# Performance work log

Hardware: AMD Instinct MI355X
Metric: run time of the kernel (lower is better)

## Reference

```python
import jax, jax.numpy as jnp
import numpy as np

GRID = 32          # grid_size -> N = 1024 patches
NPT = 1            # num_prefix_tokens
SCALE = 8.0        # sqrt(dim_head=64)
EPS = 1e-5         # nn.LayerNorm default eps


def _ln(x, g, b):
    m = jnp.mean(x, axis=-1, keepdims=True)
    v = jnp.var(x, axis=-1, keepdims=True)
    return (x - m) / jnp.sqrt(v + EPS) * g + b


def setup_inputs() -> dict:
    key = jax.random.key(0)
    ks = jax.random.split(key, 12)
    B, T, D, Dh = 32, GRID * GRID + NPT, 768, 64
    s = 0.02
    return {
        "x": jax.random.normal(ks[0], (B, T, D), jnp.float32),
        "Wq": jax.random.normal(ks[1], (D, Dh), jnp.float32) * s,
        "Wk": jax.random.normal(ks[2], (D, Dh), jnp.float32) * s,
        "Wv": jax.random.normal(ks[3], (D, Dh), jnp.float32) * s,
        "gq": jnp.ones((Dh,), jnp.float32),
        "bq": jnp.zeros((Dh,), jnp.float32),
        "gk": jnp.ones((Dh,), jnp.float32),
        "bk": jnp.zeros((Dh,), jnp.float32),
        "Wsig": jax.random.normal(ks[4], (Dh, 2), jnp.float32) * s,
        "bsig": jnp.zeros((2,), jnp.float32),
        "Wa": jax.random.normal(ks[5], (Dh, 1), jnp.float32) * s,
        "ba": jnp.zeros((1,), jnp.float32),
    }


def reference(x, Wq, Wk, Wv, gq, bq, gk, bk, Wsig, bsig, Wa, ba):
    # x: [B, T, D] with T = GRID^2 + NPT
    q = _ln(x @ Wq, gq, bq)            # [B, T, Dh]
    k = _ln(x @ Wk, gk, bk)            # [B, T, Dh]
    v = x @ Wv                          # [B, T, Dh]

    q_patch = q[:, NPT:, :]             # [B, N, Dh]
    alpha = jax.nn.softplus(q_patch @ Wa + ba)[..., 0]   # [B, N]
    sig = jax.nn.sigmoid(q_patch @ Wsig + bsig)          # [B, N, 2]
    sx, sy = sig[..., 0], sig[..., 1]                     # [B, N] each

    # patch-grid relative displacements (vectorized replacement of the
    # O(N^2) python double loop)
    ii, jj = jnp.meshgrid(jnp.arange(GRID), jnp.arange(GRID), indexing="ij")
    coords = jnp.stack([ii.ravel(), jj.ravel()], axis=-1).astype(jnp.float32)  # [N,2]=(y,x)
    dy = coords[:, None, 0] - coords[None, :, 0]          # [N, N]
    dx = coords[:, None, 1] - coords[None, :, 1]          # [N, N]

    # Gaussian bias: G[b,p,q] = exp(-dx^2/(2 sx[b,p]^2) - dy^2/(2 sy[b,p]^2))
    G = jnp.exp(-(dx * dx) / (2.0 * sx[:, :, None] ** 2)
                - (dy * dy) / (2.0 * sy[:, :, None] ** 2))  # [B, N, N]
    S = alpha[:, :, None] * G                               # [B, N, N]

    sim = jnp.einsum("bqd,bkd->bqk", q, k)                  # [B, T, T]
    sim = sim.at[:, NPT:, NPT:].add(S)

    probs = jax.nn.softmax(sim / SCALE, axis=-1)
    return probs @ v                                         # [B, T, Dh]
```

## Files before the change

### kernel.cpp

```cpp
#include <hip/hip_runtime.h>
#include <hip/hip_bf16.h>
#include <math.h>

#define BDIM 32
#define TDIM 1025
#define DDIM 768
#define GRIDW 32
#define TPATCH 1024
#define SCALE 8.0f
#define EPSLN 1e-5f
#define NROW (BDIM * TDIM)
#define VTLD 1088
#define LDP  72
#define NTILES 17

typedef __attribute__((ext_vector_type(8))) short short8v;
typedef __attribute__((ext_vector_type(4))) float f32x4;

__device__ __forceinline__ unsigned short f2bf(float f) {
    unsigned int u = __float_as_uint(f);
    u += 0x7FFFu + ((u >> 16) & 1u);
    return (unsigned short)(u >> 16);
}

__device__ __forceinline__ short8v pack8(float4 a, float4 b) {
    union { short8v v; unsigned short s[8]; } u;
    u.s[0] = f2bf(a.x); u.s[1] = f2bf(a.y); u.s[2] = f2bf(a.z); u.s[3] = f2bf(a.w);
    u.s[4] = f2bf(b.x); u.s[5] = f2bf(b.y); u.s[6] = f2bf(b.z); u.s[7] = f2bf(b.w);
    return u.v;
}

template<int CTRL>
__device__ __forceinline__ float dpp_f(float x) {
    return __int_as_float(__builtin_amdgcn_update_dpp(
        __float_as_int(x), __float_as_int(x), CTRL, 0xF, 0xF, true));
}
__device__ __forceinline__ float red16_max(float x) {
    x = fmaxf(x, dpp_f<0xB1>(x));
    x = fmaxf(x, dpp_f<0x4E>(x));
    x = fmaxf(x, dpp_f<0x124>(x));
    x = fmaxf(x, dpp_f<0x128>(x));
    return x;
}
__device__ __forceinline__ float red16_sum(float x) {
    x += dpp_f<0xB1>(x);
    x += dpp_f<0x4E>(x);
    x += dpp_f<0x124>(x);
    x += dpp_f<0x128>(x);
    return x;
}

__global__ __launch_bounds__(256) void prep_w_kernel(
    const float* __restrict__ Wq, const float* __restrict__ Wk,
    const float* __restrict__ Wv, unsigned short* __restrict__ wT)
{
    const int c = blockIdx.x;
    const float* W = (c < 64) ? Wq : (c < 128) ? Wk : Wv;
    const int cc = c & 63;
    for (int k = threadIdx.x; k < DDIM; k += 256)
        wT[(size_t)c * DDIM + k] = f2bf(W[(size_t)k * 64 + cc]);
}

__global__ __launch_bounds__(256) void qkv_tile_kernel(
    const float* __restrict__ x, const unsigned short* __restrict__ wT,
    const float* __restrict__ gq, const float* __restrict__ bq,
    const float* __restrict__ gk, const float* __restrict__ bk,
    const float* __restrict__ Wsig, const float* __restrict__ bsig,
    const float* __restrict__ Wa, const float* __restrict__ ba,
    unsigned short* __restrict__ qb, unsigned short* __restrict__ kb,
    unsigned short* __restrict__ vb,
    float* __restrict__ a8, float* __restrict__ isx, float* __restrict__ isy)
{
    __shared__ unsigned short As[2][64][LDP];
    __shared__ unsigned short Bs[2][192][LDP];

    const int t  = threadIdx.x;
    const int wv = t >> 6;
    const int ln = t & 63;
    const int lq = ln >> 4;
    const int lr = ln & 15;
    const int tok0 = blockIdx.x * 64;

    const float* la_ptr[2];
    const unsigned short* lb_ptr[6];
#pragma unroll
    for (int j = 0; j < 2; ++j) {
        int lin = t + 256 * j;
        la_ptr[j] = x + (size_t)min(tok0 + (lin >> 3), NROW - 1) * DDIM + (lin & 7) * 8;
    }
#pragma unroll
    for (int j = 0; j < 6; ++j) {
        int lin = t + 256 * j;
        lb_ptr[j] = wT + (size_t)(lin >> 3) * DDIM + (lin & 7) * 8;
    }

    float4  raf[2][2];
    short8v rbv[6];

#define QLOAD(K0)                                                              \
    do {                                                                       \
        _Pragma("unroll") for (int j = 0; j < 2; ++j) {                        \
            raf[j][0] = *(const float4*)(la_ptr[j] + (K0));                    \
            raf[j][1] = *(const float4*)(la_ptr[j] + (K0) + 4);                \
        }                                                                      \
        _Pragma("unroll") for (int j = 0; j < 6; ++j)                          \
            rbv[j] = *(const short8v*)(lb_ptr[j] + (K0));                      \
    } while (0)

#define QSTORE(BUF)                                                            \
    do {                                                                       \
        _Pragma("unroll") for (int j = 0; j < 2; ++j) {                        \
            int lin = t + 256 * j;                                             \
            *(short8v*)&As[BUF][lin >> 3][(lin & 7) * 8] =                     \
                pack8(raf[j][0], raf[j][1]);                                   \
        }                                                                      \
        _Pragma("unroll") for (int j = 0; j < 6; ++j) {                        \
            int lin = t + 256 * j;                                             \
            *(short8v*)&Bs[BUF][lin >> 3][(lin & 7) * 8] = rbv[j];             \
        }                                                                      \
    } while (0)

    f32x4 acc[12];
#pragma unroll
    for (int ni = 0; ni < 12; ++ni) acc[ni] = (f32x4){0.f, 0.f, 0.f, 0.f};

    QLOAD(0);
    QSTORE(0);
    __syncthreads();

#pragma unroll
    for (int ks = 0; ks < 12; ++ks) {
        const int buf = ks & 1;
        if (ks + 1 < 12) QLOAD((ks + 1) * 64);
        short8v af0 = *(const short8v*)&As[buf][wv * 16 + lr][lq * 8];
        short8v af1 = *(const short8v*)&As[buf][wv * 16 + lr][32 + lq * 8];
#pragma unroll
        for (int ni = 0; ni < 12; ++ni) {
            short8v bf0 = *(const short8v*)&Bs[buf][16 * ni + lr][lq * 8];
            acc[ni] = __builtin_amdgcn_mfma_f32_16x16x32_bf16(af0, bf0, acc[ni], 0, 0, 0);
            short8v bf1 = *(const short8v*)&Bs[buf][16 * ni + lr][32 + lq * 8];
            acc[ni] = __builtin_amdgcn_mfma_f32_16x16x32_bf16(af1, bf1, acc[ni], 0, 0, 0);
        }
        if (ks + 1 < 12) QSTORE(buf ^ 1);
        __syncthreads();
    }
#undef QLOAD
#undef QSTORE

    float gqv[4], bqv[4], gkv[4], bkv[4], wav[4], ws0[4], ws1[4];
#pragma unroll
    for (int ni = 0; ni < 4; ++ni) {
        int c = lr + 16 * ni;
        gqv[ni] = gq[c]; bqv[ni] = bq[c];
        gkv[ni] = gk[c]; bkv[ni] = bk[c];
        wav[ni] = Wa[c];
        ws0[ni] = Wsig[2 * c];
        ws1[ni] = Wsig[2 * c + 1];
    }
    const float ba0 = ba[0], bs0 = bsig[0], bs1 = bsig[1];

#pragma unroll
    for (int reg = 0; reg < 4; ++reg) {
        const int tokr = tok0 + wv * 16 + lq * 4 + reg;

        float s1 = 0.f, s2 = 0.f;
#pragma unroll
        for (int ni = 0; ni < 4; ++ni) {
            float v = acc[ni][reg];
            s1 += v; s2 += v * v;
        }
        s1 = red16_sum(s1);
        s2 = red16_sum(s2);
        float mean = s1 * (1.f / 64.f);
        float var  = s2 * (1.f / 64.f) - mean * mean;
        float rstd = rsqrtf(var + EPSLN);
        float qn[4];
#pragma unroll
        for (int ni = 0; ni < 4; ++ni)
            qn[ni] = (acc[ni][reg] - mean) * rstd * gqv[ni] + bqv[ni];

        s1 = 0.f; s2 = 0.f;
#pragma unroll
        for (int ni = 0; ni < 4; ++ni) {
            float v = acc[4 + ni][reg];
            s1 += v; s2 += v * v;
        }
        s1 = red16_sum(s1);
        s2 = red16_sum(s2);
        mean = s1 * (1.f / 64.f);
        var  = s2 * (1.f / 64.f) - mean * mean;
        rstd = rsqrtf(var + EPSLN);
        float kn[4];
#pragma unroll
        for (int ni = 0; ni < 4; ++ni)
            kn[ni] = (acc[4 + ni][reg] - mean) * rstd * gkv[ni] + bkv[ni];

        float da = 0.f, d0 = 0.f, d1 = 0.f;
#pragma unroll
        for (int ni = 0; ni < 4; ++ni) {
            da += qn[ni] * wav[ni];
            d0 += qn[ni] * ws0[ni];
            d1 += qn[ni] * ws1[ni];
        }
        da = red16_sum(da);
        d0 = red16_sum(d0);
        d1 = red16_sum(d1);

        if (tokr < NROW) {
            size_t base = (size_t)tokr * 64;
            int bidx = tokr / TDIM;
            int ti   = tokr - bidx * TDIM;
#pragma unroll
            for (int ni = 0; ni < 4; ++ni) {
                int c = lr + 16 * ni;
                qb[base + c] = f2bf(qn[ni]);
                kb[base + c] = f2bf(kn[ni]);
                vb[base + c] = f2bf(acc[8 + ni][reg]);
            }
            if (lr == 0 && ti >= 1) {
                int p = bidx * TPATCH + ti - 1;
                float av = da + ba0;
                float sp = (av > 20.f) ? av : log1pf(__expf(av));
                a8[p] = sp * (1.f / SCALE);
                float sx = 1.f / (1.f + __expf(-(d0 + bs0)));
                float sy = 1.f / (1.f + __expf(-(d1 + bs1)));
                isx[p] = 0.5f / (sx * sx);
                isy[p] = 0.5f / (sy * sy);
            }
        }
    }
}

__global__ __launch_bounds__(256) void vtrans_kernel(
    const unsigned short* __restrict__ vb, unsigned short* __restrict__ vT)
{
    __shared__ unsigned short tile[64][LDP];
    const int t  = threadIdx.x;
    const int bb = blockIdx.y;
    const int t0 = blockIdx.x * 64;

#pragma unroll
    for (int it = 0; it < 2; ++it) {
        int lin = t + it * 256;
        int tok = lin >> 3;
        int d0  = (lin & 7) * 8;
        short8v v8 = {0, 0, 0, 0, 0, 0, 0, 0};
        if (t0 + tok < TDIM)
            v8 = *(const short8v*)&vb[((size_t)bb * TDIM + t0 + tok) * 64 + d0];
        union { short8v v; unsigned short s[8]; } u; u.v = v8;
#pragma unroll
        for (int j = 0; j < 8; ++j) tile[d0 + j][tok] = u.s[j];
    }
    __syncthreads();

    const int dh = t >> 2;
    const int ch = t & 3;
    short8v o0 = *(const short8v*)&tile[dh][ch * 16];
    short8v o1 = *(const short8v*)&tile[dh][ch * 16 + 8];
    size_t dst = ((size_t)bb * 64 + dh) * VTLD + t0 + ch * 16;
    *(short8v*)&vT[dst]     = o0;
    *(short8v*)&vT[dst + 8] = o1;
}

__global__ __launch_bounds__(256) void attn_mfma_kernel(
    const unsigned short* __restrict__ qb, const unsigned short* __restrict__ kb,
    const unsigned short* __restrict__ vT,
    const float* __restrict__ a8, const float* __restrict__ isx,
    const float* __restrict__ isy, float* __restrict__ out)
{
    __shared__ unsigned short Ks[2][64][LDP];
    __shared__ unsigned short Vt[2][64][LDP];
    __shared__ unsigned short Pt[4][16][LDP];

    const int t  = threadIdx.x;
    const int wv = t >> 6;
    const int ln = t & 63;
    const int lq = ln >> 4;
    const int lr = ln & 15;
    const int bb = blockIdx.y;
    const int q0 = blockIdx.x * 64;

    const int qrow = min(q0 + wv * 16 + lr, TDIM - 1);
    const size_t qbase = ((size_t)bb * TDIM + qrow) * 64;
    const short8v aq0 = *(const short8v*)&qb[qbase + lq * 8];
    const short8v aq1 = *(const short8v*)&qb[qbase + 32 + lq * 8];

    float a8q[4], sxq[4], syq[4], qpy[4], qpx[4];
    bool  hasS[4];
#pragma unroll
    for (int reg = 0; reg < 4; ++reg) {
        int qg = q0 + wv * 16 + lq * 4 + reg;
        hasS[reg] = false;
        a8q[reg] = 0.f; sxq[reg] = 0.f; syq[reg] = 0.f; qpy[reg] = 0.f; qpx[reg] = 0.f;
        if (qg >= 1 && qg < TDIM) {
            int qp = qg - 1;
            hasS[reg] = true;
            a8q[reg] = a8 [bb * TPATCH + qp];
            sxq[reg] = isx[bb * TPATCH + qp];
            syq[reg] = isy[bb * TPATCH + qp];
            qpy[reg] = (float)(qp >> 5);
            qpx[reg] = (float)(qp & 31);
        }
    }

    float m[4]  = {-1e30f, -1e30f, -1e30f, -1e30f};
    float l[4]  = {0.f, 0.f, 0.f, 0.f};
    f32x4 oacc[4];
#pragma unroll
    for (int ni = 0; ni < 4; ++ni) oacc[ni] = (f32x4){0.f, 0.f, 0.f, 0.f};

    const int sk_row = t >> 3;
    const int sk_d0  = (t & 7) * 8;
    short8v rk[2], rv[2];

#define ALOAD(KT0)                                                             \
    do {                                                                       \
        _Pragma("unroll") for (int it = 0; it < 2; ++it) {                     \
            int key = sk_row + 32 * it;                                        \
            int kg  = (KT0) + key;                                             \
            rk[it] = (kg < TDIM)                                               \
                ? *(const short8v*)&kb[((size_t)bb * TDIM + kg) * 64 + sk_d0]  \
                : (short8v){0, 0, 0, 0, 0, 0, 0, 0};                           \
            rv[it] = *(const short8v*)&vT[((size_t)bb * 64 + key) * VTLD +     \
                                          (KT0) + sk_d0];                      \
        }                                                                      \
    } while (0)

#define ASTORE(BUF)                                                            \
    do {                                                                       \
        _Pragma("unroll") for (int it = 0; it < 2; ++it) {                     \
            *(short8v*)&Ks[BUF][sk_row + 32 * it][sk_d0] = rk[it];             \
            *(short8v*)&Vt[BUF][sk_row + 32 * it][sk_d0] = rv[it];             \
        }                                                                      \
    } while (0)

    ALOAD(0);
    ASTORE(0);
    __syncthreads();

    for (int tile = 0; tile < NTILES; ++tile) {
        const int kt0 = tile * 64;
        const int buf = tile & 1;
        if (tile + 1 < NTILES) ALOAD(kt0 + 64);

        f32x4 sac[4];
#pragma unroll
        for (int ni = 0; ni < 4; ++ni) sac[ni] = (f32x4){0.f, 0.f, 0.f, 0.f};
#pragma unroll
        for (int ni = 0; ni < 4; ++ni) {
            short8v b0 = *(const short8v*)&Ks[buf][16 * ni + lr][lq * 8];
            short8v b1 = *(const short8v*)&Ks[buf][16 * ni + lr][32 + lq * 8];
            sac[ni] = __builtin_amdgcn_mfma_f32_16x16x32_bf16(aq0, b0, sac[ni], 0, 0, 0);
            sac[ni] = __builtin_amdgcn_mfma_f32_16x16x32_bf16(aq1, b1, sac[ni], 0, 0, 0);
        }

#pragma unroll
        for (int ni = 0; ni < 4; ++ni) {
            int key = kt0 + 16 * ni + lr;
            int kp  = key - 1;
            float ky = (float)(kp >> 5);
            float kx = (float)(kp & 31);
            bool kvalid = (key >= 1) && (key < TDIM);
#pragma unroll
            for (int reg = 0; reg < 4; ++reg) {
                float z = sac[ni][reg] * (1.f / SCALE);
                if (kvalid && hasS[reg]) {
                    float dy = qpy[reg] - ky;
                    float dx = qpx[reg] - kx;
                    z += a8q[reg] * __expf(-(dx * dx * sxq[reg] + dy * dy * syq[reg]));
                }
                if (key >= TDIM) z = -1e30f;
                sac[ni][reg] = z;
            }
        }

        float scf[4];
#pragma unroll
        for (int reg = 0; reg < 4; ++reg) {
            float mx = fmaxf(fmaxf(sac[0][reg], sac[1][reg]),
                             fmaxf(sac[2][reg], sac[3][reg]));
            mx = red16_max(mx);
            float mn = fmaxf(m[reg], mx);
            scf[reg] = __expf(m[reg] - mn);
            m[reg] = mn;
            float ts = 0.f;
#pragma unroll
            for (int ni = 0; ni < 4; ++ni) {
                float pp = __expf(sac[ni][reg] - mn);
                sac[ni][reg] = pp;
                ts += pp;
            }
            ts = red16_sum(ts);
            l[reg] = l[reg] * scf[reg] + ts;
        }
#pragma unroll
        for (int ni = 0; ni < 4; ++ni)
#pragma unroll
            for (int reg = 0; reg < 4; ++reg)
                oacc[ni][reg] *= scf[reg];

#pragma unroll
        for (int ni = 0; ni < 4; ++ni)
#pragma unroll
            for (int reg = 0; reg < 4; ++reg)
                Pt[wv][lq * 4 + reg][16 * ni + lr] = f2bf(sac[ni][reg]);

#pragma unroll
        for (int ks = 0; ks < 2; ++ks) {
            short8v pa = *(const short8v*)&Pt[wv][lr][ks * 32 + lq * 8];
#pragma unroll
            for (int ni = 0; ni < 4; ++ni) {
                short8v bv = *(const short8v*)&Vt[buf][16 * ni + lr][ks * 32 + lq * 8];
                oacc[ni] = __builtin_amdgcn_mfma_f32_16x16x32_bf16(pa, bv, oacc[ni], 0, 0, 0);
            }
        }

        if (tile + 1 < NTILES) ASTORE(buf ^ 1);
        __syncthreads();
    }
#undef ALOAD
#undef ASTORE

#pragma unroll
    for (int reg = 0; reg < 4; ++reg) {
        int qg = q0 + wv * 16 + lq * 4 + reg;
        if (qg < TDIM) {
            float rl = 1.f / l[reg];
#pragma unroll
            for (int ni = 0; ni < 4; ++ni)
                out[((size_t)bb * TDIM + qg) * 64 + 16 * ni + lr] = oacc[ni][reg] * rl;
        }
    }
}

extern "C" void kernel_launch(void* const* d_in, const int* in_sizes, int n_in,
                              void* d_out, int out_size, void* d_ws, size_t ws_size,
                              hipStream_t stream)
{
    const float* x    = (const float*)d_in[0];
    const float* Wq   = (const float*)d_in[1];
    const float* Wk   = (const float*)d_in[2];
    const float* Wv   = (const float*)d_in[3];
    const float* gq   = (const float*)d_in[4];
    const float* bq   = (const float*)d_in[5];
    const float* gk   = (const float*)d_in[6];
    const float* bk   = (const float*)d_in[7];
    const float* Wsig = (const float*)d_in[8];
    const float* bsig = (const float*)d_in[9];
    const float* Wa   = (const float*)d_in[10];
    const float* ba   = (const float*)d_in[11];
    float* out = (float*)d_out;

    char* w = (char*)d_ws;
    const size_t NQ = (size_t)NROW * 64;
    unsigned short* qb = (unsigned short*)w;   w += NQ * 2;
    unsigned short* kb = (unsigned short*)w;   w += NQ * 2;
    unsigned short* vb = (unsigned short*)w;   w += NQ * 2;
    unsigned short* vT = (unsigned short*)w;   w += (size_t)BDIM * 64 * VTLD * 2;
    float* a8  = (float*)w;                    w += (size_t)BDIM * TPATCH * 4;
    float* isx = (float*)w;                    w += (size_t)BDIM * TPATCH * 4;
    float* isy = (float*)w;                    w += (size_t)BDIM * TPATCH * 4;
    unsigned short* wT = (unsigned short*)w;   w += (size_t)192 * DDIM * 2;

    hipLaunchKernelGGL(prep_w_kernel, dim3(192), dim3(256), 0, stream,
                       Wq, Wk, Wv, wT);

    const int nblk1 = (NROW + 63) / 64;
    hipLaunchKernelGGL(qkv_tile_kernel, dim3(nblk1), dim3(256), 0, stream,
                       x, wT, gq, bq, gk, bk, Wsig, bsig, Wa, ba,
                       qb, kb, vb, a8, isx, isy);

    hipLaunchKernelGGL(vtrans_kernel, dim3(17, BDIM), dim3(256), 0, stream,
                       vb, vT);

    hipLaunchKernelGGL(attn_mfma_kernel, dim3(17, BDIM), dim3(256), 0, stream,
                       qb, kb, vT, a8, isx, isy, out);
}
```

Measured before the change: 108.5 us.

## Halve QKV GEMM K-tile and double-buffer register prefetch with lighter barriers

The QKV projection GEMM now steps through K in 32-wide slices instead of 64, using narrower shared tiles. Two alternating register prefetch sets keep a global load two slices ahead of the MFMA compute. Both the QKV and attention kernels replace __syncthreads with a barrier that waits only on LDS counters and adds a scheduling fence, so outstanding global loads can stay in flight across it. The aim is better overlap of global memory traffic with MFMA work, at the cost of twice as many barriers in the GEMM and more live registers.

```diff
diff --git a/kernel.cpp b/kernel.cpp
--- a/kernel.cpp
+++ b/kernel.cpp
@@ -12,6 +12,7 @@
 #define NROW (BDIM * TDIM)
 #define VTLD 1088
 #define LDP  72
+#define LDQ  40
 #define NTILES 17
 
 typedef __attribute__((ext_vector_type(8))) short short8v;
@@ -23,11 +24,16 @@
     return (unsigned short)(u >> 16);
 }
 
-__device__ __forceinline__ short8v pack8(float4 a, float4 b) {
-    union { short8v v; unsigned short s[8]; } u;
-    u.s[0] = f2bf(a.x); u.s[1] = f2bf(a.y); u.s[2] = f2bf(a.z); u.s[3] = f2bf(a.w);
-    u.s[4] = f2bf(b.x); u.s[5] = f2bf(b.y); u.s[6] = f2bf(b.z); u.s[7] = f2bf(b.w);
-    return u.v;
+__device__ __forceinline__ ushort4 pack4(float4 a) {
+    ushort4 r;
+    r.x = f2bf(a.x); r.y = f2bf(a.y); r.z = f2bf(a.z); r.w = f2bf(a.w);
+    return r;
+}
+
+__device__ __forceinline__ void wg_barrier() {
+    asm volatile("s_waitcnt lgkmcnt(0)" ::: "memory");
+    __builtin_amdgcn_s_barrier();
+    __builtin_amdgcn_sched_barrier(0);
 }
 
 template<int CTRL>
@@ -71,8 +77,8 @@
     unsigned short* __restrict__ vb,
     float* __restrict__ a8, float* __restrict__ isx, float* __restrict__ isy)
 {
-    __shared__ unsigned short As[2][64][LDP];
-    __shared__ unsigned short Bs[2][192][LDP];
+    __shared__ unsigned short As[2][64][LDQ];
+    __shared__ unsigned short Bs[2][192][LDQ];
 
     const int t  = threadIdx.x;
     const int wv = t >> 6;
@@ -81,71 +87,87 @@
     const int lr = ln & 15;
     const int tok0 = blockIdx.x * 64;
 
-    const float* la_ptr[2];
-    const unsigned short* lb_ptr[6];
-#pragma unroll
-    for (int j = 0; j < 2; ++j) {
-        int lin = t + 256 * j;
-        la_ptr[j] = x + (size_t)min(tok0 + (lin >> 3), NROW - 1) * DDIM + (lin & 7) * 8;
-    }
-#pragma unroll
-    for (int j = 0; j < 6; ++j) {
-        int lin = t + 256 * j;
-        lb_ptr[j] = wT + (size_t)(lin >> 3) * DDIM + (lin & 7) * 8;
-    }
-
-    float4  raf[2][2];
-    short8v rbv[6];
-
-#define QLOAD(K0)                                                              \
-    do {                                                                       \
-        _Pragma("unroll") for (int j = 0; j < 2; ++j) {                        \
-            raf[j][0] = *(const float4*)(la_ptr[j] + (K0));                    \
-            raf[j][1] = *(const float4*)(la_ptr[j] + (K0) + 4);                \
+    const int ar0 = t >> 3,          as0 = (t & 7) * 4;
+    const int ar1 = (t + 256) >> 3,  as1 = ((t + 256) & 7) * 4;
+    const float* la0 = x + (size_t)min(tok0 + ar0, NROW - 1) * DDIM + as0;
+    const float* la1 = x + (size_t)min(tok0 + ar1, NROW - 1) * DDIM + as1;
+    const int br0 = t >> 2,          bs0 = (t & 3) * 8;
+    const int br1 = (t + 256) >> 2,  bs1 = ((t + 256) & 3) * 8;
+    const int br2 = (t + 512) >> 2,  bs2 = ((t + 512) & 3) * 8;
+    const unsigned short* lb0 = wT + (size_t)br0 * DDIM + bs0;
+    const unsigned short* lb1 = wT + (size_t)br1 * DDIM + bs1;
+    const unsigned short* lb2 = wT + (size_t)br2 * DDIM + bs2;
+
+    float4  raA0, raA1, raB0, raB1;
+    short8v rbA0, rbA1, rbA2, rbB0, rbB1, rbB2;
+
+#define LOAD_SET_A(K0)                                                         \
+    do {                                                                       \
+        raA0 = *(const float4*)(la0 + (K0));                                   \
+        raA1 = *(const float4*)(la1 + (K0));                                   \
+        rbA0 = *(const short8v*)(lb0 + (K0));                                  \
+        rbA1 = *(const short8v*)(lb1 + (K0));                                  \
+        rbA2 = *(const short8v*)(lb2 + (K0));                                  \
+    } while (0)
+#define LOAD_SET_B(K0)                                                         \
+    do {                                                                       \
+        raB0 = *(const float4*)(la0 + (K0));                                   \
+        raB1 = *(const float4*)(la1 + (K0));                                   \
+        rbB0 = *(const short8v*)(lb0 + (K0));                                  \
+        rbB1 = *(const short8v*)(lb1 + (K0));                                  \
+        rbB2 = *(const short8v*)(lb2 + (K0));                                  \
+    } while (0)
+#define STORE_SET_A()                                                          \
+    do {                                                                       \
+        *(ushort4*)&As[0][ar0][as0] = pack4(raA0);                             \
+        *(ushort4*)&As[0][ar1][as1] = pack4(raA1);                             \
+        *(short8v*)&Bs[0][br0][bs0] = rbA0;                                    \
+        *(short8v*)&Bs[0][br1][bs1] = rbA1;                                    \
+        *(short8v*)&Bs[0][br2][bs2] = rbA2;                                    \
+    } while (0)
+#define STORE_SET_B()                                                          \
+    do {                                                                       \
+        *(ushort4*)&As[1][ar0][as0] = pack4(raB0);                             \
+        *(ushort4*)&As[1][ar1][as1] = pack4(raB1);                             \
+        *(short8v*)&Bs[1][br0][bs0] = rbB0;                                    \
+        *(short8v*)&Bs[1][br1][bs1] = rbB1;                                    \
+        *(short8v*)&Bs[1][br2][bs2] = rbB2;                                    \
+    } while (0)
+#define COMPUTE(BUF)                                                           \
+    do {                                                                       \
+        short8v af = *(const short8v*)&As[BUF][wv * 16 + lr][lq * 8];          \
+        _Pragma("unroll") for (int ni = 0; ni < 12; ++ni) {                    \
+            short8v bf = *(const short8v*)&Bs[BUF][16 * ni + lr][lq * 8];      \
+            acc[ni] = __builtin_amdgcn_mfma_f32_16x16x32_bf16(af, bf,          \
+                                                              acc[ni], 0, 0, 0); \
         }                                                                      \
-        _Pragma("unroll") for (int j = 0; j < 6; ++j)                          \
-            rbv[j] = *(const short8v*)(lb_ptr[j] + (K0));                      \
-    } while (0)
-
-#define QSTORE(BUF)                                                            \
-    do {                                                                       \
-        _Pragma("unroll") for (int j = 0; j < 2; ++j) {                        \
-            int lin = t + 256 * j;                                             \
-            *(short8v*)&As[BUF][lin >> 3][(lin & 7) * 8] =                     \
-                pack8(raf[j][0], raf[j][1]);                                   \
-        }                                                                      \
-        _Pragma("unroll") for (int j = 0; j < 6; ++j) {                        \
-            int lin = t + 256 * j;                                             \
-            *(short8v*)&Bs[BUF][lin >> 3][(lin & 7) * 8] = rbv[j];             \
-        }                                                                      \
     } while (0)
 
     f32x4 acc[12];
 #pragma unroll
     for (int ni = 0; ni < 12; ++ni) acc[ni] = (f32x4){0.f, 0.f, 0.f, 0.f};
 
-    QLOAD(0);
-    QSTORE(0);
-    __syncthreads();
-
-#pragma unroll
-    for (int ks = 0; ks < 12; ++ks) {
-        const int buf = ks & 1;
-        if (ks + 1 < 12) QLOAD((ks + 1) * 64);
-        short8v af0 = *(const short8v*)&As[buf][wv * 16 + lr][lq * 8];
-        short8v af1 = *(const short8v*)&As[buf][wv * 16 + lr][32 + lq * 8];
-#pragma unroll
-        for (int ni = 0; ni < 12; ++ni) {
-            short8v bf0 = *(const short8v*)&Bs[buf][16 * ni + lr][lq * 8];
-            acc[ni] = __builtin_amdgcn_mfma_f32_16x16x32_bf16(af0, bf0, acc[ni], 0, 0, 0);
-            short8v bf1 = *(const short8v*)&Bs[buf][16 * ni + lr][32 + lq * 8];
-            acc[ni] = __builtin_amdgcn_mfma_f32_16x16x32_bf16(af1, bf1, acc[ni], 0, 0, 0);
-        }
-        if (ks + 1 < 12) QSTORE(buf ^ 1);
-        __syncthreads();
-    }
-#undef QLOAD
-#undef QSTORE
+    LOAD_SET_A(0);
+    LOAD_SET_B(32);
+    STORE_SET_A();
+    wg_barrier();
+
+#pragma unroll
+    for (int ks = 0; ks < 24; ks += 2) {
+        if (ks + 2 < 24) LOAD_SET_A((ks + 2) * 32);
+        COMPUTE(0);
+        STORE_SET_B();
+        wg_barrier();
+        if (ks + 3 < 24) LOAD_SET_B((ks + 3) * 32);
+        COMPUTE(1);
+        if (ks + 2 < 24) STORE_SET_A();
+        wg_barrier();
+    }
+#undef LOAD_SET_A
+#undef LOAD_SET_B
+#undef STORE_SET_A
+#undef STORE_SET_B
+#undef COMPUTE
 
     float gqv[4], bqv[4], gkv[4], bkv[4], wav[4], ws0[4], ws1[4];
 #pragma unroll
@@ -157,7 +179,7 @@
         ws0[ni] = Wsig[2 * c];
         ws1[ni] = Wsig[2 * c + 1];
     }
-    const float ba0 = ba[0], bs0 = bsig[0], bs1 = bsig[1];
+    const float ba0 = ba[0], bs0c = bsig[0], bs1c = bsig[1];
 
 #pragma unroll
     for (int reg = 0; reg < 4; ++reg) {
@@ -222,8 +244,8 @@
                 float av = da + ba0;
                 float sp = (av > 20.f) ? av : log1pf(__expf(av));
                 a8[p] = sp * (1.f / SCALE);
-                float sx = 1.f / (1.f + __expf(-(d0 + bs0)));
-                float sy = 1.f / (1.f + __expf(-(d1 + bs1)));
+                float sx = 1.f / (1.f + __expf(-(d0 + bs0c)));
+                float sy = 1.f / (1.f + __expf(-(d1 + bs1c)));
                 isx[p] = 0.5f / (sx * sx);
                 isy[p] = 0.5f / (sy * sy);
             }
@@ -336,7 +358,7 @@
 
     ALOAD(0);
     ASTORE(0);
-    __syncthreads();
+    wg_barrier();
 
     for (int tile = 0; tile < NTILES; ++tile) {
         const int kt0 = tile * 64;
@@ -416,7 +438,7 @@
         }
 
         if (tile + 1 < NTILES) ASTORE(buf ^ 1);
-        __syncthreads();
+        wg_barrier();
     }
 #undef ALOAD
 #undef ASTORE
```

After: 95.55 us. 12.0% less time.

## Restructure QKV projection into single-wave 32-token blocks without barriers

Applied to the files above, without the earlier changes.

The QKV projection kernel moves from 256-thread blocks over 64 tokens with double-buffered LDS to 64-thread single-wave blocks over 32 tokens. Each wave computes two 16-row M tiles against all 192 output columns with a K step of 32. Because only one wave shares the LDS tiles, the per-step workgroup barriers are removed and a single buffer is enough. This doubles the number of blocks and the re-reads of the weight tile, and relies on each wave covering enough latency on its own. The attention kernel's __syncthreads is also replaced by an explicit lgkmcnt wait, s_barrier and scheduling barrier.

```diff
diff --git a/kernel.cpp b/kernel.cpp
--- a/kernel.cpp
+++ b/kernel.cpp
@@ -12,6 +12,7 @@
 #define NROW (BDIM * TDIM)
 #define VTLD 1088
 #define LDP  72
+#define LDQ  40
 #define NTILES 17
 
 typedef __attribute__((ext_vector_type(8))) short short8v;
@@ -23,11 +24,16 @@
     return (unsigned short)(u >> 16);
 }
 
-__device__ __forceinline__ short8v pack8(float4 a, float4 b) {
-    union { short8v v; unsigned short s[8]; } u;
-    u.s[0] = f2bf(a.x); u.s[1] = f2bf(a.y); u.s[2] = f2bf(a.z); u.s[3] = f2bf(a.w);
-    u.s[4] = f2bf(b.x); u.s[5] = f2bf(b.y); u.s[6] = f2bf(b.z); u.s[7] = f2bf(b.w);
-    return u.v;
+__device__ __forceinline__ ushort4 pack4(float4 a) {
+    ushort4 r;
+    r.x = f2bf(a.x); r.y = f2bf(a.y); r.z = f2bf(a.z); r.w = f2bf(a.w);
+    return r;
+}
+
+__device__ __forceinline__ void wg_barrier() {
+    asm volatile("s_waitcnt lgkmcnt(0)" ::: "memory");
+    __builtin_amdgcn_s_barrier();
+    __builtin_amdgcn_sched_barrier(0);
 }
 
 template<int CTRL>
@@ -61,7 +67,7 @@
         wT[(size_t)c * DDIM + k] = f2bf(W[(size_t)k * 64 + cc]);
 }
 
-__global__ __launch_bounds__(256) void qkv_tile_kernel(
+__global__ __launch_bounds__(64) void qkv_tile_kernel(
     const float* __restrict__ x, const unsigned short* __restrict__ wT,
     const float* __restrict__ gq, const float* __restrict__ bq,
     const float* __restrict__ gk, const float* __restrict__ bk,
@@ -71,78 +77,72 @@
     unsigned short* __restrict__ vb,
     float* __restrict__ a8, float* __restrict__ isx, float* __restrict__ isy)
 {
-    __shared__ unsigned short As[2][64][LDP];
-    __shared__ unsigned short Bs[2][192][LDP];
-
-    const int t  = threadIdx.x;
-    const int wv = t >> 6;
-    const int ln = t & 63;
-    const int lq = ln >> 4;
-    const int lr = ln & 15;
-    const int tok0 = blockIdx.x * 64;
-
-    const float* la_ptr[2];
-    const unsigned short* lb_ptr[6];
-#pragma unroll
-    for (int j = 0; j < 2; ++j) {
-        int lin = t + 256 * j;
-        la_ptr[j] = x + (size_t)min(tok0 + (lin >> 3), NROW - 1) * DDIM + (lin & 7) * 8;
-    }
-#pragma unroll
-    for (int j = 0; j < 6; ++j) {
-        int lin = t + 256 * j;
-        lb_ptr[j] = wT + (size_t)(lin >> 3) * DDIM + (lin & 7) * 8;
-    }
-
-    float4  raf[2][2];
-    short8v rbv[6];
+    __shared__ unsigned short As[32][LDQ];
+    __shared__ unsigned short Bs[192][LDQ];
+
+    const int l  = threadIdx.x;
+    const int lq = l >> 4;
+    const int lr = l & 15;
+    const int tok0 = blockIdx.x * 32;
+
+    const float* aptr[4];
+    int arow[4], aseg[4];
+#pragma unroll
+    for (int j = 0; j < 4; ++j) {
+        int c = l + 64 * j;
+        arow[j] = c >> 3;
+        aseg[j] = (c & 7) * 4;
+        aptr[j] = x + (size_t)(tok0 + arow[j]) * DDIM + aseg[j];
+    }
+    const unsigned short* bptr[12];
+    int brow[12], bseg[12];
+#pragma unroll
+    for (int j = 0; j < 12; ++j) {
+        int c = l + 64 * j;
+        brow[j] = c >> 2;
+        bseg[j] = (c & 3) * 8;
+        bptr[j] = wT + (size_t)brow[j] * DDIM + bseg[j];
+    }
+
+    float4  ra[4];
+    short8v rb[12];
 
 #define QLOAD(K0)                                                              \
     do {                                                                       \
-        _Pragma("unroll") for (int j = 0; j < 2; ++j) {                        \
-            raf[j][0] = *(const float4*)(la_ptr[j] + (K0));                    \
-            raf[j][1] = *(const float4*)(la_ptr[j] + (K0) + 4);                \
-        }                                                                      \
-        _Pragma("unroll") for (int j = 0; j < 6; ++j)                          \
-            rbv[j] = *(const short8v*)(lb_ptr[j] + (K0));                      \
+        _Pragma("unroll") for (int j = 0; j < 4; ++j)                          \
+            ra[j] = *(const float4*)(aptr[j] + (K0));                          \
+        _Pragma("unroll") for (int j = 0; j < 12; ++j)                         \
+            rb[j] = *(const short8v*)(bptr[j] + (K0));                         \
     } while (0)
-
-#define QSTORE(BUF)                                                            \
+#define QSTORE()                                                               \
     do {                                                                       \
-        _Pragma("unroll") for (int j = 0; j < 2; ++j) {                        \
-            int lin = t + 256 * j;                                             \
-            *(short8v*)&As[BUF][lin >> 3][(lin & 7) * 8] =                     \
-                pack8(raf[j][0], raf[j][1]);                                   \
-        }                                                                      \
-        _Pragma("unroll") for (int j = 0; j < 6; ++j) {                        \
-            int lin = t + 256 * j;                                             \
-            *(short8v*)&Bs[BUF][lin >> 3][(lin & 7) * 8] = rbv[j];             \
-        }                                                                      \
+        _Pragma("unroll") for (int j = 0; j < 4; ++j)                          \
+            *(ushort4*)&As[arow[j]][aseg[j]] = pack4(ra[j]);                   \
+        _Pragma("unroll") for (int j = 0; j < 12; ++j)                         \
+            *(short8v*)&Bs[brow[j]][bseg[j]] = rb[j];                          \
     } while (0)
 
-    f32x4 acc[12];
-#pragma unroll
-    for (int ni = 0; ni < 12; ++ni) acc[ni] = (f32x4){0.f, 0.f, 0.f, 0.f};
+    f32x4 acc[2][12];
+#pragma unroll
+    for (int mi = 0; mi < 2; ++mi)
+#pragma unroll
+        for (int ni = 0; ni < 12; ++ni)
+            acc[mi][ni] = (f32x4){0.f, 0.f, 0.f, 0.f};
 
     QLOAD(0);
-    QSTORE(0);
-    __syncthreads();
-
-#pragma unroll
-    for (int ks = 0; ks < 12; ++ks) {
-        const int buf = ks & 1;
-        if (ks + 1 < 12) QLOAD((ks + 1) * 64);
-        short8v af0 = *(const short8v*)&As[buf][wv * 16 + lr][lq * 8];
-        short8v af1 = *(const short8v*)&As[buf][wv * 16 + lr][32 + lq * 8];
+    QSTORE();
+
+    for (int ks = 0; ks < 24; ++ks) {
+        if (ks + 1 < 24) QLOAD((ks + 1) * 32);
+        short8v af0 = *(const short8v*)&As[ 0 + lr][lq * 8];
+        short8v af1 = *(const short8v*)&As[16 + lr][lq * 8];
 #pragma unroll
         for (int ni = 0; ni < 12; ++ni) {
-            short8v bf0 = *(const short8v*)&Bs[buf][16 * ni + lr][lq * 8];
-            acc[ni] = __builtin_amdgcn_mfma_f32_16x16x32_bf16(af0, bf0, acc[ni], 0, 0, 0);
-            short8v bf1 = *(const short8v*)&Bs[buf][16 * ni + lr][32 + lq * 8];
-            acc[ni] = __builtin_amdgcn_mfma_f32_16x16x32_bf16(af1, bf1, acc[ni], 0, 0, 0);
-        }
-        if (ks + 1 < 12) QSTORE(buf ^ 1);
-        __syncthreads();
+            short8v bf = *(const short8v*)&Bs[16 * ni + lr][lq * 8];
+            acc[0][ni] = __builtin_amdgcn_mfma_f32_16x16x32_bf16(af0, bf, acc[0][ni], 0, 0, 0);
+            acc[1][ni] = __builtin_amdgcn_mfma_f32_16x16x32_bf16(af1, bf, acc[1][ni], 0, 0, 0);
+        }
+        if (ks + 1 < 24) QSTORE();
     }
 #undef QLOAD
 #undef QSTORE
@@ -157,16 +157,18 @@
         ws0[ni] = Wsig[2 * c];
         ws1[ni] = Wsig[2 * c + 1];
     }
-    const float ba0 = ba[0], bs0 = bsig[0], bs1 = bsig[1];
-
+    const float ba0 = ba[0], bs0c = bsig[0], bs1c = bsig[1];
+
+#pragma unroll
+    for (int mi = 0; mi < 2; ++mi) {
 #pragma unroll
     for (int reg = 0; reg < 4; ++reg) {
-        const int tokr = tok0 + wv * 16 + lq * 4 + reg;
+        const int tokr = tok0 + mi * 16 + lq * 4 + reg;
 
         float s1 = 0.f, s2 = 0.f;
 #pragma unroll
         for (int ni = 0; ni < 4; ++ni) {
-            float v = acc[ni][reg];
+            float v = acc[mi][ni][reg];
             s1 += v; s2 += v * v;
         }
         s1 = red16_sum(s1);
@@ -177,12 +179,12 @@
         float qn[4];
 #pragma unroll
         for (int ni = 0; ni < 4; ++ni)
-            qn[ni] = (acc[ni][reg] - mean) * rstd * gqv[ni] + bqv[ni];
+            qn[ni] = (acc[mi][ni][reg] - mean) * rstd * gqv[ni] + bqv[ni];
 
         s1 = 0.f; s2 = 0.f;
 #pragma unroll
         for (int ni = 0; ni < 4; ++ni) {
-            float v = acc[4 + ni][reg];
+            float v = acc[mi][4 + ni][reg];
             s1 += v; s2 += v * v;
         }
         s1 = red16_sum(s1);
@@ -193,7 +195,7 @@
         float kn[4];
 #pragma unroll
         for (int ni = 0; ni < 4; ++ni)
-            kn[ni] = (acc[4 + ni][reg] - mean) * rstd * gkv[ni] + bkv[ni];
+            kn[ni] = (acc[mi][4 + ni][reg] - mean) * rstd * gkv[ni] + bkv[ni];
 
         float da = 0.f, d0 = 0.f, d1 = 0.f;
 #pragma unroll
@@ -206,7 +208,7 @@
         d0 = red16_sum(d0);
         d1 = red16_sum(d1);
 
-        if (tokr < NROW) {
+        {
             size_t base = (size_t)tokr * 64;
             int bidx = tokr / TDIM;
             int ti   = tokr - bidx * TDIM;
@@ -215,19 +217,20 @@
                 int c = lr + 16 * ni;
                 qb[base + c] = f2bf(qn[ni]);
                 kb[base + c] = f2bf(kn[ni]);
-                vb[base + c] = f2bf(acc[8 + ni][reg]);
+                vb[base + c] = f2bf(acc[mi][8 + ni][reg]);
             }
             if (lr == 0 && ti >= 1) {
                 int p = bidx * TPATCH + ti - 1;
                 float av = da + ba0;
                 float sp = (av > 20.f) ? av : log1pf(__expf(av));
                 a8[p] = sp * (1.f / SCALE);
-                float sx = 1.f / (1.f + __expf(-(d0 + bs0)));
-                float sy = 1.f / (1.f + __expf(-(d1 + bs1)));
+                float sx = 1.f / (1.f + __expf(-(d0 + bs0c)));
+                float sy = 1.f / (1.f + __expf(-(d1 + bs1c)));
                 isx[p] = 0.5f / (sx * sx);
                 isy[p] = 0.5f / (sy * sy);
             }
         }
+    }
     }
 }
 
@@ -336,7 +339,7 @@
 
     ALOAD(0);
     ASTORE(0);
-    __syncthreads();
+    wg_barrier();
 
     for (int tile = 0; tile < NTILES; ++tile) {
         const int kt0 = tile * 64;
@@ -416,7 +419,7 @@
         }
 
         if (tile + 1 < NTILES) ASTORE(buf ^ 1);
-        __syncthreads();
+        wg_barrier();
     }
 #undef ALOAD
 #undef ASTORE
@@ -465,8 +468,8 @@
     hipLaunchKernelGGL(prep_w_kernel, dim3(192), dim3(256), 0, stream,
                        Wq, Wk, Wv, wT);
 
-    const int nblk1 = (NROW + 63) / 64;
-    hipLaunchKernelGGL(qkv_tile_kernel, dim3(nblk1), dim3(256), 0, stream,
+    const int nblk1 = NROW / 32;
+    hipLaunchKernelGGL(qkv_tile_kernel, dim3(nblk1), dim3(64), 0, stream,
                        x, wT, gq, bq, gk, bk, Wsig, bsig, Wa, ba,
                        qb, kb, vb, a8, isx, isy);
 
```

Measured after the change: 105.4 us (median of 2 runs). 1.03x faster.

## Load x directly into MFMA fragments and stage weights in large LDS chunks

Applied to the files above, without the earlier changes.

The QKV projection kernel no longer stages x through LDS. Each lane loads its own x row segment straight from global memory into registers, converts it to bf16 for the MFMA operand, and prefetches two steps ahead. The weight matrix is staged in three 256-wide K chunks with a single buffer, which cuts the number of barriers from twelve to six, but loads and compute no longer overlap within a chunk. The attention kernel's __syncthreads calls are replaced by a custom barrier that waits only on lgkmcnt and adds a scheduling barrier. That barrier does not wait on outstanding global loads.

```diff
diff --git a/kernel.cpp b/kernel.cpp
--- a/kernel.cpp
+++ b/kernel.cpp
@@ -12,6 +12,8 @@
 #define NROW (BDIM * TDIM)
 #define VTLD 1088
 #define LDP  72
+#define BKC  256
+#define LDB  264
 #define NTILES 17
 
 typedef __attribute__((ext_vector_type(8))) short short8v;
@@ -28,6 +30,12 @@
     u.s[0] = f2bf(a.x); u.s[1] = f2bf(a.y); u.s[2] = f2bf(a.z); u.s[3] = f2bf(a.w);
     u.s[4] = f2bf(b.x); u.s[5] = f2bf(b.y); u.s[6] = f2bf(b.z); u.s[7] = f2bf(b.w);
     return u.v;
+}
+
+__device__ __forceinline__ void wg_barrier() {
+    asm volatile("s_waitcnt lgkmcnt(0)" ::: "memory");
+    __builtin_amdgcn_s_barrier();
+    __builtin_amdgcn_sched_barrier(0);
 }
 
 template<int CTRL>
@@ -61,7 +69,7 @@
         wT[(size_t)c * DDIM + k] = f2bf(W[(size_t)k * 64 + cc]);
 }
 
-__global__ __launch_bounds__(256) void qkv_tile_kernel(
+__global__ __launch_bounds__(256) void qkv_bstat_kernel(
     const float* __restrict__ x, const unsigned short* __restrict__ wT,
     const float* __restrict__ gq, const float* __restrict__ bq,
     const float* __restrict__ gk, const float* __restrict__ bk,
@@ -71,81 +79,59 @@
     unsigned short* __restrict__ vb,
     float* __restrict__ a8, float* __restrict__ isx, float* __restrict__ isy)
 {
-    __shared__ unsigned short As[2][64][LDP];
-    __shared__ unsigned short Bs[2][192][LDP];
+    __shared__ unsigned short Bs[192][LDB];
 
     const int t  = threadIdx.x;
     const int wv = t >> 6;
     const int ln = t & 63;
     const int lq = ln >> 4;
     const int lr = ln & 15;
-    const int tok0 = blockIdx.x * 64;
-
-    const float* la_ptr[2];
-    const unsigned short* lb_ptr[6];
-#pragma unroll
-    for (int j = 0; j < 2; ++j) {
-        int lin = t + 256 * j;
-        la_ptr[j] = x + (size_t)min(tok0 + (lin >> 3), NROW - 1) * DDIM + (lin & 7) * 8;
-    }
-#pragma unroll
-    for (int j = 0; j < 6; ++j) {
-        int lin = t + 256 * j;
-        lb_ptr[j] = wT + (size_t)(lin >> 3) * DDIM + (lin & 7) * 8;
-    }
-
-    float4  raf[2][2];
-    short8v rbv[6];
-
-#define QLOAD(K0)                                                              \
-    do {                                                                       \
-        _Pragma("unroll") for (int j = 0; j < 2; ++j) {                        \
-            raf[j][0] = *(const float4*)(la_ptr[j] + (K0));                    \
-            raf[j][1] = *(const float4*)(la_ptr[j] + (K0) + 4);                \
-        }                                                                      \
-        _Pragma("unroll") for (int j = 0; j < 6; ++j)                          \
-            rbv[j] = *(const short8v*)(lb_ptr[j] + (K0));                      \
-    } while (0)
-
-#define QSTORE(BUF)                                                            \
-    do {                                                                       \
-        _Pragma("unroll") for (int j = 0; j < 2; ++j) {                        \
-            int lin = t + 256 * j;                                             \
-            *(short8v*)&As[BUF][lin >> 3][(lin & 7) * 8] =                     \
-                pack8(raf[j][0], raf[j][1]);                                   \
-        }                                                                      \
-        _Pragma("unroll") for (int j = 0; j < 6; ++j) {                        \
-            int lin = t + 256 * j;                                             \
-            *(short8v*)&Bs[BUF][lin >> 3][(lin & 7) * 8] = rbv[j];             \
-        }                                                                      \
-    } while (0)
+    const int tokb = blockIdx.x * 64 + wv * 16;
+
+    const float* xrow = x + (size_t)min(tokb + lr, NROW - 1) * DDIM + lq * 8;
 
     f32x4 acc[12];
 #pragma unroll
     for (int ni = 0; ni < 12; ++ni) acc[ni] = (f32x4){0.f, 0.f, 0.f, 0.f};
 
-    QLOAD(0);
-    QSTORE(0);
-    __syncthreads();
-
-#pragma unroll
-    for (int ks = 0; ks < 12; ++ks) {
-        const int buf = ks & 1;
-        if (ks + 1 < 12) QLOAD((ks + 1) * 64);
-        short8v af0 = *(const short8v*)&As[buf][wv * 16 + lr][lq * 8];
-        short8v af1 = *(const short8v*)&As[buf][wv * 16 + lr][32 + lq * 8];
-#pragma unroll
-        for (int ni = 0; ni < 12; ++ni) {
-            short8v bf0 = *(const short8v*)&Bs[buf][16 * ni + lr][lq * 8];
-            acc[ni] = __builtin_amdgcn_mfma_f32_16x16x32_bf16(af0, bf0, acc[ni], 0, 0, 0);
-            short8v bf1 = *(const short8v*)&Bs[buf][16 * ni + lr][32 + lq * 8];
-            acc[ni] = __builtin_amdgcn_mfma_f32_16x16x32_bf16(af1, bf1, acc[ni], 0, 0, 0);
-        }
-        if (ks + 1 < 12) QSTORE(buf ^ 1);
-        __syncthreads();
-    }
-#undef QLOAD
-#undef QSTORE
+    float4 a00, a01, a10, a11;
+    a00 = *(const float4*)(xrow + 0);
+    a01 = *(const float4*)(xrow + 4);
+    a10 = *(const float4*)(xrow + 32);
+    a11 = *(const float4*)(xrow + 36);
+
+#pragma unroll
+    for (int kc = 0; kc < 3; ++kc) {
+#pragma unroll
+        for (int j = 0; j < 24; ++j) {
+            int idx = t + 256 * j;
+            int row = idx >> 5;
+            int seg = idx & 31;
+            short8v v = *(const short8v*)&wT[(size_t)row * DDIM + kc * BKC + seg * 8];
+            *(short8v*)&Bs[row][seg * 8] = v;
+        }
+        wg_barrier();
+
+#pragma unroll
+        for (int ks = 0; ks < 8; ++ks) {
+            const int s = kc * 8 + ks;
+            float4 n0, n1;
+            const bool pf = (s + 2 < 24);
+            if (pf) {
+                n0 = *(const float4*)(xrow + (s + 2) * 32);
+                n1 = *(const float4*)(xrow + (s + 2) * 32 + 4);
+            }
+            short8v af = pack8(a00, a01);
+#pragma unroll
+            for (int ni = 0; ni < 12; ++ni) {
+                short8v bf = *(const short8v*)&Bs[16 * ni + lr][ks * 32 + lq * 8];
+                acc[ni] = __builtin_amdgcn_mfma_f32_16x16x32_bf16(af, bf, acc[ni], 0, 0, 0);
+            }
+            a00 = a10; a01 = a11;
+            if (pf) { a10 = n0; a11 = n1; }
+        }
+        wg_barrier();
+    }
 
     float gqv[4], bqv[4], gkv[4], bkv[4], wav[4], ws0[4], ws1[4];
 #pragma unroll
@@ -157,11 +143,11 @@
         ws0[ni] = Wsig[2 * c];
         ws1[ni] = Wsig[2 * c + 1];
     }
-    const float ba0 = ba[0], bs0 = bsig[0], bs1 = bsig[1];
+    const float ba0 = ba[0], bs0c = bsig[0], bs1c = bsig[1];
 
 #pragma unroll
     for (int reg = 0; reg < 4; ++reg) {
-        const int tokr = tok0 + wv * 16 + lq * 4 + reg;
+        const int tokr = tokb + lq * 4 + reg;
 
         float s1 = 0.f, s2 = 0.f;
 #pragma unroll
@@ -222,8 +208,8 @@
                 float av = da + ba0;
                 float sp = (av > 20.f) ? av : log1pf(__expf(av));
                 a8[p] = sp * (1.f / SCALE);
-                float sx = 1.f / (1.f + __expf(-(d0 + bs0)));
-                float sy = 1.f / (1.f + __expf(-(d1 + bs1)));
+                float sx = 1.f / (1.f + __expf(-(d0 + bs0c)));
+                float sy = 1.f / (1.f + __expf(-(d1 + bs1c)));
                 isx[p] = 0.5f / (sx * sx);
                 isy[p] = 0.5f / (sy * sy);
             }
@@ -336,7 +322,7 @@
 
     ALOAD(0);
     ASTORE(0);
-    __syncthreads();
+    wg_barrier();
 
     for (int tile = 0; tile < NTILES; ++tile) {
         const int kt0 = tile * 64;
@@ -416,7 +402,7 @@
         }
 
         if (tile + 1 < NTILES) ASTORE(buf ^ 1);
-        __syncthreads();
+        wg_barrier();
     }
 #undef ALOAD
 #undef ASTORE
@@ -466,7 +452,7 @@
                        Wq, Wk, Wv, wT);
 
     const int nblk1 = (NROW + 63) / 64;
-    hipLaunchKernelGGL(qkv_tile_kernel, dim3(nblk1), dim3(256), 0, stream,
+    hipLaunchKernelGGL(qkv_bstat_kernel, dim3(nblk1), dim3(256), 0, stream,
                        x, wT, gq, bq, gk, bk, Wsig, bsig, Wa, ba,
                        qb, kb, vb, a8, isx, isy);
 
```

New measurement: 124.1 us. 14.4% more time.
